# Kernel tuning notes

Measured on AMD Instinct MI355X. Metric: run time of the kernel, lower is better.

## Reference

```python
import jax, jax.numpy as jnp
import numpy as np

DENSE_SHAPE = (256, 3, 3, 256)  # (out_channels, kh, kw, in_channels)
STRIDES = (1, 1)


def _unfold_nchw(x, kh, kw, sh, sw):
    """torch.nn.functional.unfold layout: rows ordered (C, kh, kw)."""
    B, C, H, W = x.shape
    oh = (H - kh) // sh + 1
    ow = (W - kw) // sw + 1
    # [B, C, kh*kw, oh, ow]; small python loop over 3x3 kernel taps only
    patches = jnp.stack(
        [x[:, :, i:i + sh * oh:sh, j:j + sw * ow:sw]
         for i in range(kh) for j in range(kw)], axis=2)
    return patches.reshape(B, C * kh * kw, oh * ow), oh, ow


def setup_inputs() -> dict:
    key = jax.random.key(0)
    k1, k2, k3, k4, k5, k6 = jax.random.split(key, 6)
    O, kh, kw, C = DENSE_SHAPE
    nnz = 2048
    inp = jax.random.normal(k1, (4, 128, 128, C), dtype=jnp.float32)
    # per-column index ranges for COO weight indices [nnz, 4]
    io = jax.random.randint(k2, (nnz, 1), 0, O)
    ih = jax.random.randint(k3, (nnz, 1), 0, kh)
    iw = jax.random.randint(k4, (nnz, 1), 0, kw)
    ic = jax.random.randint(k5, (nnz, 1), 0, C)
    weight_indices = jnp.concatenate([io, ih, iw, ic], axis=1).astype(jnp.int64)
    weight_values = jax.random.normal(k6, (nnz,), dtype=jnp.float32)
    return {"input": inp, "weight_indices": weight_indices,
            "weight_values": weight_values}


def reference(input, weight_indices, weight_values):
    O, kh, kw, C = DENSE_SHAPE
    sh, sw = STRIDES
    B = input.shape[0]
    # densify COO weight (duplicates are summed, matching coalesce)
    W = jnp.zeros(DENSE_SHAPE, dtype=weight_values.dtype).at[
        weight_indices[:, 0], weight_indices[:, 1],
        weight_indices[:, 2], weight_indices[:, 3]].add(weight_values)
    x = jnp.transpose(input, (0, 3, 1, 2))  # NHWC -> NCHW
    U, oh, ow = _unfold_nchw(x, kh, kw, sh, sw)  # [B, C*kh*kw, oh*ow]
    # NOTE: faithful to the original: weight flattened in (kh,kw,C) order
    # while unfold rows are in (C,kh,kw) order -- same raw matmul.
    out = jnp.einsum('ok,bkl->bol', W.reshape(O, -1), U)
    out = out.reshape(B, O, oh, ow)
    return jnp.transpose(out, (0, 2, 3, 1))  # -> NHWC
```

## Files before the change

### kernel.cpp

```cpp
#include <hip/hip_runtime.h>
#include <cstdint>

#define H_IN   128
#define W_IN   128
#define C_IN   256
#define O_OUT  256
#define OH     126
#define OW     126

#define TY     8
#define TX     8
#define IR     (TY + 2)
#define ICOLS  (TX + 2)
#define NPIX   (IR * ICOLS)
#define COLB   516
#define ROWB   5264
#define IN_BYTES (9 * ROWB + 9 * COLB + COLB)
#define NWAVES 16
#define OPW    16
#define SST    18
#define STG_W  (64 * SST)
#define FLUSH_BYTES (8 * STG_W * 4)
#define LDS_BYTES IN_BYTES

__global__ void prep_kernel(const int* __restrict__ wi, const float* __restrict__ wv,
                            int nnz, int* __restrict__ sgS, int* __restrict__ sgBase,
                            int* __restrict__ perm, int2* __restrict__ tab) {
    __shared__ int cnt[256];
    __shared__ int ipos[256];
    __shared__ int prm[256];
    __shared__ int hist[64];
    __shared__ int hbase[65];
    __shared__ int hcur[64];
    __shared__ int smax[32];
    __shared__ int sbase[33];
    __shared__ int is32;
    const int tid = threadIdx.x;
    cnt[tid] = 0;
    if (tid < 64) { hist[tid] = 0; hcur[tid] = 0; }
    if (tid == 0) is32 = 0;
    __syncthreads();
    int f = 0;
    for (int idx = tid * 2 + 1; idx < nnz * 4; idx += 512) f |= wi[idx];
    if (f) atomicOr(&is32, 1);
    __syncthreads();
    const int stride = is32 ? 4 : 8;
    const int step   = is32 ? 1 : 2;
    for (int e = tid; e < nnz; e += 256)
        atomicAdd(&cnt[wi[e * stride]], 1);
    __syncthreads();
    { int key = 63 - min(cnt[tid], 63); atomicAdd(&hist[key], 1); }
    __syncthreads();
    if (tid == 0) {
        int s = 0;
        for (int i = 0; i < 64; ++i) { hbase[i] = s; s += hist[i]; }
        hbase[64] = s;
    }
    __syncthreads();
    { int key = 63 - min(cnt[tid], 63);
      int pos = hbase[key] + atomicAdd(&hcur[key], 1);
      ipos[tid] = pos; prm[pos] = tid; }
    __syncthreads();
    if (tid < 32) {
        int m = 0;
        for (int k = 0; k < 8; ++k) m = max(m, cnt[prm[tid * 8 + k]]);
        smax[tid] = m;
    }
    __syncthreads();
    if (tid == 0) {
        int s = 0;
        for (int i = 0; i < 32; ++i) { sbase[i] = s; s += 8 * smax[i]; }
        sbase[32] = s;
    }
    __syncthreads();
    const int T = sbase[32];
    for (int i = tid; i < T; i += 256) tab[i] = make_int2(0, 0);
    cnt[tid] = 0;
    __syncthreads();
    for (int e = tid; e < nnz; e += 256) {
        int o  = wi[e * stride];
        int h  = wi[e * stride + 1 * step];
        int w_ = wi[e * stride + 2 * step];
        int c  = wi[e * stride + 3 * step];
        int k   = h * 768 + w_ * 256 + c;
        int cp  = k / 9;
        int rem = k - cp * 9;
        int i_  = rem / 3;
        int j_  = rem - i_ * 3;
        int meta2 = i_ * ROWB + j_ * COLB + cp * 2;
        int slot = atomicAdd(&cnt[o], 1);
        int p    = ipos[o];
        tab[sbase[p >> 3] + slot * 8 + (p & 7)] = make_int2(meta2, __float_as_int(wv[e]));
    }
    if (tid < 32) sgS[tid] = smax[tid];
    if (tid < 33) sgBase[tid] = sbase[tid];
    perm[tid] = prm[tid];
}

__device__ inline unsigned short rtne_bf16(float f) {
    unsigned u = __float_as_uint(f);
    u += 0x7FFFu + ((u >> 16) & 1u);
    return (unsigned short)(u >> 16);
}

__device__ __forceinline__ float bfld(const char* b, int off) {
    return __uint_as_float(((unsigned)*(const unsigned short*)(b + off)) << 16);
}

__global__ __launch_bounds__(1024, 8)
void conv_kernel(const float* __restrict__ in, float* __restrict__ out,
                 const int* __restrict__ sgS, const int* __restrict__ sgBase,
                 const int* __restrict__ perm, const int2* __restrict__ tab) {
    extern __shared__ char smem[];
    float* ldsF = (float*)smem;

    const int tid  = threadIdx.x;
    const int w    = __builtin_amdgcn_readfirstlane(tid >> 6);
    const int lane = tid & 63;
    const int tx = blockIdx.x, ty = blockIdx.y, b = blockIdx.z;
    const int iy0 = ty * TY, ix0 = tx * TX;
    const float* inb = in + (size_t)b * (H_IN * W_IN * C_IN);

    for (int base = 0; base < 8; base += 4) {
        float4 v[4];
#pragma unroll
        for (int q = 0; q < 4; ++q) {
            int p = w + (base + q) * NWAVES;
            if (p < NPIX) {
                int r = p / ICOLS, c = p - r * ICOLS;
                int gy = iy0 + r, gx = ix0 + c;
                if (gy < H_IN && gx < W_IN)
                    v[q] = *(const float4*)(inb + ((gy * W_IN + gx) << 8) + (lane << 2));
            }
        }
#pragma unroll
        for (int q = 0; q < 4; ++q) {
            int p = w + (base + q) * NWAVES;
            if (p < NPIX) {
                int r = p / ICOLS, c = p - r * ICOLS;
                int gy = iy0 + r, gx = ix0 + c;
                if (gy < H_IN && gx < W_IN) {
                    ushort2 lo, hi;
                    lo.x = rtne_bf16(v[q].x); lo.y = rtne_bf16(v[q].y);
                    hi.x = rtne_bf16(v[q].z); hi.y = rtne_bf16(v[q].w);
                    unsigned short* d = (unsigned short*)(smem + r * ROWB + c * COLB) + (lane << 2);
                    *(ushort2*)(d)     = lo;
                    *(ushort2*)(d + 2) = hi;
                }
            }
        }
    }
    __syncthreads();

    const int A2  = (lane >> 3) * ROWB + (lane & 7) * COLB;
    const int g0 = w, g1 = 31 - w;
    const char* basep = (const char*)smem;
    float acc[OPW];
#pragma unroll
    for (int i = 0; i < OPW; ++i) acc[i] = 0.f;

#pragma unroll
    for (int g = 0; g < 2; ++g) {
        const int gi = g ? g1 : g0;
        const int S = sgS[gi];
        const int2* Tg = tab + sgBase[gi];
        for (int slot = 0; slot < S; ++slot) {
            const int4* R = (const int4*)(Tg + (slot << 3));
            const int4 p0 = R[0];
            const int4 p1 = R[1];
            const int4 p2 = R[2];
            const int4 p3 = R[3];
            acc[g * 8 + 0] += __int_as_float(p0.y) * bfld(basep, A2 + p0.x);
            acc[g * 8 + 1] += __int_as_float(p0.w) * bfld(basep, A2 + p0.z);
            acc[g * 8 + 2] += __int_as_float(p1.y) * bfld(basep, A2 + p1.x);
            acc[g * 8 + 3] += __int_as_float(p1.w) * bfld(basep, A2 + p1.z);
            acc[g * 8 + 4] += __int_as_float(p2.y) * bfld(basep, A2 + p2.x);
            acc[g * 8 + 5] += __int_as_float(p2.w) * bfld(basep, A2 + p2.z);
            acc[g * 8 + 6] += __int_as_float(p3.y) * bfld(basep, A2 + p3.x);
            acc[g * 8 + 7] += __int_as_float(p3.w) * bfld(basep, A2 + p3.z);
        }
    }

    __syncthreads();
    int tcs[OPW];
#pragma unroll
    for (int k = 0; k < OPW; ++k) {
        const int grp = (k < 8) ? g0 : g1;
        tcs[k] = perm[grp * 8 + (k & 7)];
    }
    const int ob = w * OPW;
#pragma unroll
    for (int k = 0; k < OPW; ++k) {
        const int tc = tcs[k];
        if ((tc >> 7) == 0)
            ldsF[((tc >> 4) & 7) * STG_W + lane * SST + (tc & 15)] = acc[k];
    }
    __syncthreads();
    if (w < 8) {
        const int a_  = lane >> 2;
        const int chq = lane & 3;
        const float* rb = ldsF + w * STG_W;
#pragma unroll
        for (int s16 = 0; s16 < 4; ++s16) {
            int p = s16 * 16 + a_;
            float2 u0 = *(const float2*)(rb + p * SST + chq * 4);
            float2 u1 = *(const float2*)(rb + p * SST + chq * 4 + 2);
            int poy = iy0 + (p >> 3), pox = ix0 + (p & 7);
            if (poy < OH && pox < OW) {
                float4 o4 = make_float4(u0.x, u0.y, u1.x, u1.y);
                *(float4*)(out + (((size_t)b * OH + poy) * OW + pox) * O_OUT + ob + chq * 4) = o4;
            }
        }
    }
    __syncthreads();
#pragma unroll
    for (int k = 0; k < OPW; ++k) {
        const int tc = tcs[k];
        if ((tc >> 7) == 1)
            ldsF[((tc >> 4) & 7) * STG_W + lane * SST + (tc & 15)] = acc[k];
    }
    __syncthreads();
    if (w >= 8) {
        const int a_  = lane >> 2;
        const int chq = lane & 3;
        const float* rb = ldsF + (w & 7) * STG_W;
#pragma unroll
        for (int s16 = 0; s16 < 4; ++s16) {
            int p = s16 * 16 + a_;
            float2 u0 = *(const float2*)(rb + p * SST + chq * 4);
            float2 u1 = *(const float2*)(rb + p * SST + chq * 4 + 2);
            int poy = iy0 + (p >> 3), pox = ix0 + (p & 7);
            if (poy < OH && pox < OW) {
                float4 o4 = make_float4(u0.x, u0.y, u1.x, u1.y);
                *(float4*)(out + (((size_t)b * OH + poy) * OW + pox) * O_OUT + ob + chq * 4) = o4;
            }
        }
    }
}

extern "C" void kernel_launch(void* const* d_in, const int* in_sizes, int n_in,
                              void* d_out, int out_size, void* d_ws, size_t ws_size,
                              hipStream_t stream) {
    const float* input = (const float*)d_in[0];
    const int*   widx  = (const int*)d_in[1];
    const float* wval  = (const float*)d_in[2];
    float* outp = (float*)d_out;
    const int nnz = in_sizes[2];
    const int B = in_sizes[0] / (H_IN * W_IN * C_IN);

    int*  sgS    = (int*)d_ws;
    int*  sgBase = sgS + 32;
    int*  perm   = (int*)((char*)d_ws + 512);
    int2* tab    = (int2*)((char*)d_ws + 2048);

    prep_kernel<<<1, 256, 0, stream>>>(widx, wval, nnz, sgS, sgBase, perm, tab);

    static_assert(LDS_BYTES >= FLUSH_BYTES, "flush pass must fit in input region");
    static_assert(2 * LDS_BYTES <= 160 * 1024, "need 2 blocks/CU");
    hipFuncSetAttribute((const void*)conv_kernel,
                        hipFuncAttributeMaxDynamicSharedMemorySize, LDS_BYTES);
    dim3 grid((OW + TX - 1) / TX, (OH + TY - 1) / TY, B);
    conv_kernel<<<grid, 1024, LDS_BYTES, stream>>>(input, outp, sgS, sgBase, perm, tab);
}
```

Baseline: 140.9 us.

## Swizzle block order, prefetch weight table rows, spread output flush across all waves

Remaps the flat block index so that consecutively launched blocks land on different batch and tile positions, changing L2 and channel locality. The sparse-weight table loop now software-prefetches the next slot's entries while computing the current one, hiding the table load latency behind LDS reads and FMAs. The output flush is restructured so all 16 waves write every stage instead of half idling, each lane storing two float4s per pixel. This adds register pressure from the prefetched int4s and relies on the swizzle matching the grid shape (16x16x4).

```diff
diff --git a/kernel.cpp b/kernel.cpp
--- a/kernel.cpp
+++ b/kernel.cpp
@@ -117,7 +117,9 @@
     const int tid  = threadIdx.x;
     const int w    = __builtin_amdgcn_readfirstlane(tid >> 6);
     const int lane = tid & 63;
-    const int tx = blockIdx.x, ty = blockIdx.y, b = blockIdx.z;
+    const int flat = ((int)blockIdx.z << 8) | ((int)blockIdx.y << 4) | (int)blockIdx.x;
+    const int swz  = ((flat & 7) << 7) | (flat >> 3);
+    const int tx = swz & 15, ty = (swz >> 4) & 15, b = swz >> 8;
     const int iy0 = ty * TY, ix0 = tx * TX;
     const float* inb = in + (size_t)b * (H_IN * W_IN * C_IN);
 
@@ -153,7 +155,6 @@
     __syncthreads();
 
     const int A2  = (lane >> 3) * ROWB + (lane & 7) * COLB;
-    const int g0 = w, g1 = 31 - w;
     const char* basep = (const char*)smem;
     float acc[OPW];
 #pragma unroll
@@ -161,23 +162,28 @@
 
 #pragma unroll
     for (int g = 0; g < 2; ++g) {
-        const int gi = g ? g1 : g0;
+        const int gi = g ? (31 - w) : w;
         const int S = sgS[gi];
-        const int2* Tg = tab + sgBase[gi];
-        for (int slot = 0; slot < S; ++slot) {
-            const int4* R = (const int4*)(Tg + (slot << 3));
-            const int4 p0 = R[0];
-            const int4 p1 = R[1];
-            const int4 p2 = R[2];
-            const int4 p3 = R[3];
-            acc[g * 8 + 0] += __int_as_float(p0.y) * bfld(basep, A2 + p0.x);
-            acc[g * 8 + 1] += __int_as_float(p0.w) * bfld(basep, A2 + p0.z);
-            acc[g * 8 + 2] += __int_as_float(p1.y) * bfld(basep, A2 + p1.x);
-            acc[g * 8 + 3] += __int_as_float(p1.w) * bfld(basep, A2 + p1.z);
-            acc[g * 8 + 4] += __int_as_float(p2.y) * bfld(basep, A2 + p2.x);
-            acc[g * 8 + 5] += __int_as_float(p2.w) * bfld(basep, A2 + p2.z);
-            acc[g * 8 + 6] += __int_as_float(p3.y) * bfld(basep, A2 + p3.x);
-            acc[g * 8 + 7] += __int_as_float(p3.w) * bfld(basep, A2 + p3.z);
+        if (S > 0) {
+            const int2* Tg = tab + sgBase[gi];
+            int4 c0 = ((const int4*)Tg)[0];
+            int4 c1 = ((const int4*)Tg)[1];
+            int4 c2 = ((const int4*)Tg)[2];
+            int4 c3 = ((const int4*)Tg)[3];
+            for (int slot = 0; slot < S; ++slot) {
+                const int nxt = (slot + 1 < S) ? (slot + 1) : slot;
+                const int4* Rn = (const int4*)(Tg + (nxt << 3));
+                int4 n0 = Rn[0], n1 = Rn[1], n2 = Rn[2], n3 = Rn[3];
+                acc[g * 8 + 0] += __int_as_float(c0.y) * bfld(basep, A2 + c0.x);
+                acc[g * 8 + 1] += __int_as_float(c0.w) * bfld(basep, A2 + c0.z);
+                acc[g * 8 + 2] += __int_as_float(c1.y) * bfld(basep, A2 + c1.x);
+                acc[g * 8 + 3] += __int_as_float(c1.w) * bfld(basep, A2 + c1.z);
+                acc[g * 8 + 4] += __int_as_float(c2.y) * bfld(basep, A2 + c2.x);
+                acc[g * 8 + 5] += __int_as_float(c2.w) * bfld(basep, A2 + c2.z);
+                acc[g * 8 + 6] += __int_as_float(c3.y) * bfld(basep, A2 + c3.x);
+                acc[g * 8 + 7] += __int_as_float(c3.w) * bfld(basep, A2 + c3.z);
+                c0 = n0; c1 = n1; c2 = n2; c3 = n3;
+            }
         }
     }
 
@@ -185,10 +191,16 @@
     int tcs[OPW];
 #pragma unroll
     for (int k = 0; k < OPW; ++k) {
-        const int grp = (k < 8) ? g0 : g1;
+        const int grp = (k < 8) ? w : (31 - w);
         tcs[k] = perm[grp * 8 + (k & 7)];
     }
-    const int ob = w * OPW;
+    const int rq   = w >> 1;
+    const int rpx  = (w & 1) * 32 + (lane >> 1);
+    const int half = lane & 1;
+    const int poy  = iy0 + (rpx >> 3), pox = ix0 + (rpx & 7);
+    const float* rb = ldsF + rq * STG_W + rpx * SST + half * 8;
+    float* outp0 = out + (((size_t)b * OH + poy) * OW + pox) * O_OUT + rq * 16 + half * 8;
+    const bool inb_px = (poy < OH) && (pox < OW);
 #pragma unroll
     for (int k = 0; k < OPW; ++k) {
         const int tc = tcs[k];
@@ -196,20 +208,14 @@
             ldsF[((tc >> 4) & 7) * STG_W + lane * SST + (tc & 15)] = acc[k];
     }
     __syncthreads();
-    if (w < 8) {
-        const int a_  = lane >> 2;
-        const int chq = lane & 3;
-        const float* rb = ldsF + w * STG_W;
-#pragma unroll
-        for (int s16 = 0; s16 < 4; ++s16) {
-            int p = s16 * 16 + a_;
-            float2 u0 = *(const float2*)(rb + p * SST + chq * 4);
-            float2 u1 = *(const float2*)(rb + p * SST + chq * 4 + 2);
-            int poy = iy0 + (p >> 3), pox = ix0 + (p & 7);
-            if (poy < OH && pox < OW) {
-                float4 o4 = make_float4(u0.x, u0.y, u1.x, u1.y);
-                *(float4*)(out + (((size_t)b * OH + poy) * OW + pox) * O_OUT + ob + chq * 4) = o4;
-            }
+    {
+        float2 u0 = *(const float2*)(rb + 0);
+        float2 u1 = *(const float2*)(rb + 2);
+        float2 u2 = *(const float2*)(rb + 4);
+        float2 u3 = *(const float2*)(rb + 6);
+        if (inb_px) {
+            *(float4*)(outp0 + 0) = make_float4(u0.x, u0.y, u1.x, u1.y);
+            *(float4*)(outp0 + 4) = make_float4(u2.x, u2.y, u3.x, u3.y);
         }
     }
     __syncthreads();
@@ -220,20 +226,14 @@
             ldsF[((tc >> 4) & 7) * STG_W + lane * SST + (tc & 15)] = acc[k];
     }
     __syncthreads();
-    if (w >= 8) {
-        const int a_  = lane >> 2;
-        const int chq = lane & 3;
-        const float* rb = ldsF + (w & 7) * STG_W;
-#pragma unroll
-        for (int s16 = 0; s16 < 4; ++s16) {
-            int p = s16 * 16 + a_;
-            float2 u0 = *(const float2*)(rb + p * SST + chq * 4);
-            float2 u1 = *(const float2*)(rb + p * SST + chq * 4 + 2);
-            int poy = iy0 + (p >> 3), pox = ix0 + (p & 7);
-            if (poy < OH && pox < OW) {
-                float4 o4 = make_float4(u0.x, u0.y, u1.x, u1.y);
-                *(float4*)(out + (((size_t)b * OH + poy) * OW + pox) * O_OUT + ob + chq * 4) = o4;
-            }
+    {
+        float2 u0 = *(const float2*)(rb + 0);
+        float2 u1 = *(const float2*)(rb + 2);
+        float2 u2 = *(const float2*)(rb + 4);
+        float2 u3 = *(const float2*)(rb + 6);
+        if (inb_px) {
+            *(float4*)(outp0 + 128 + 0) = make_float4(u0.x, u0.y, u1.x, u1.y);
+            *(float4*)(outp0 + 128 + 4) = make_float4(u2.x, u2.y, u3.x, u3.y);
         }
     }
 }
```

New measurement: 142.6 us. About the same (+1.2%).

## Single-pass output flush, swizzle block order, hoist permutation loads

Applied to the files above, without the earlier changes.

Replaces the two-phase staged output write with one pass: all 16 waves stage their accumulators into a larger LDS region (16 x 1156 floats), then each thread writes 64 contiguous bytes of one pixel's output. This removes two barriers and a serialized half-idle store phase. Block indices are remapped with a swizzle so consecutive blocks land on different tiles/batches, and the perm lookups are hoisted before the input load to hide their latency. LDS usage grows (~74KB per block), which still allows 2 blocks/CU but tightens the budget.

```diff
diff --git a/kernel.cpp b/kernel.cpp
--- a/kernel.cpp
+++ b/kernel.cpp
@@ -18,10 +18,10 @@
 #define IN_BYTES (9 * ROWB + 9 * COLB + COLB)
 #define NWAVES 16
 #define OPW    16
-#define SST    18
-#define STG_W  (64 * SST)
-#define FLUSH_BYTES (8 * STG_W * 4)
-#define LDS_BYTES IN_BYTES
+#define SSTW   18
+#define REGW   1156
+#define FLUSH_BYTES (16 * REGW * 4)
+#define LDS_BYTES FLUSH_BYTES
 
 __global__ void prep_kernel(const int* __restrict__ wi, const float* __restrict__ wv,
                             int nnz, int* __restrict__ sgS, int* __restrict__ sgBase,
@@ -117,9 +117,17 @@
     const int tid  = threadIdx.x;
     const int w    = __builtin_amdgcn_readfirstlane(tid >> 6);
     const int lane = tid & 63;
-    const int tx = blockIdx.x, ty = blockIdx.y, b = blockIdx.z;
+    const int flat = ((int)blockIdx.z << 8) | ((int)blockIdx.y << 4) | (int)blockIdx.x;
+    const int swz  = ((flat & 7) << 7) | (flat >> 3);
+    const int tx = swz & 15, ty = (swz >> 4) & 15, b = swz >> 8;
     const int iy0 = ty * TY, ix0 = tx * TX;
     const float* inb = in + (size_t)b * (H_IN * W_IN * C_IN);
+
+    const int g0 = w, g1 = 31 - w;
+    int tcs[OPW];
+#pragma unroll
+    for (int k = 0; k < OPW; ++k)
+        tcs[k] = perm[((k < 8) ? g0 : g1) * 8 + (k & 7)];
 
     for (int base = 0; base < 8; base += 4) {
         float4 v[4];
@@ -153,7 +161,6 @@
     __syncthreads();
 
     const int A2  = (lane >> 3) * ROWB + (lane & 7) * COLB;
-    const int g0 = w, g1 = 31 - w;
     const char* basep = (const char*)smem;
     float acc[OPW];
 #pragma unroll
@@ -182,58 +189,31 @@
     }
 
     __syncthreads();
-    int tcs[OPW];
-#pragma unroll
-    for (int k = 0; k < OPW; ++k) {
-        const int grp = (k < 8) ? g0 : g1;
-        tcs[k] = perm[grp * 8 + (k & 7)];
-    }
-    const int ob = w * OPW;
 #pragma unroll
     for (int k = 0; k < OPW; ++k) {
         const int tc = tcs[k];
-        if ((tc >> 7) == 0)
-            ldsF[((tc >> 4) & 7) * STG_W + lane * SST + (tc & 15)] = acc[k];
-    }
-    __syncthreads();
-    if (w < 8) {
-        const int a_  = lane >> 2;
-        const int chq = lane & 3;
-        const float* rb = ldsF + w * STG_W;
-#pragma unroll
-        for (int s16 = 0; s16 < 4; ++s16) {
-            int p = s16 * 16 + a_;
-            float2 u0 = *(const float2*)(rb + p * SST + chq * 4);
-            float2 u1 = *(const float2*)(rb + p * SST + chq * 4 + 2);
-            int poy = iy0 + (p >> 3), pox = ix0 + (p & 7);
-            if (poy < OH && pox < OW) {
-                float4 o4 = make_float4(u0.x, u0.y, u1.x, u1.y);
-                *(float4*)(out + (((size_t)b * OH + poy) * OW + pox) * O_OUT + ob + chq * 4) = o4;
-            }
-        }
-    }
-    __syncthreads();
-#pragma unroll
-    for (int k = 0; k < OPW; ++k) {
-        const int tc = tcs[k];
-        if ((tc >> 7) == 1)
-            ldsF[((tc >> 4) & 7) * STG_W + lane * SST + (tc & 15)] = acc[k];
-    }
-    __syncthreads();
-    if (w >= 8) {
-        const int a_  = lane >> 2;
-        const int chq = lane & 3;
-        const float* rb = ldsF + (w & 7) * STG_W;
-#pragma unroll
-        for (int s16 = 0; s16 < 4; ++s16) {
-            int p = s16 * 16 + a_;
-            float2 u0 = *(const float2*)(rb + p * SST + chq * 4);
-            float2 u1 = *(const float2*)(rb + p * SST + chq * 4 + 2);
-            int poy = iy0 + (p >> 3), pox = ix0 + (p & 7);
-            if (poy < OH && pox < OW) {
-                float4 o4 = make_float4(u0.x, u0.y, u1.x, u1.y);
-                *(float4*)(out + (((size_t)b * OH + poy) * OW + pox) * O_OUT + ob + chq * 4) = o4;
-            }
+        ldsF[(tc >> 4) * REGW + lane * SSTW + (tc & 15)] = acc[k];
+    }
+    __syncthreads();
+    {
+        const int px = tid >> 4;
+        const int q  = tid & 15;
+        const int poy = iy0 + (px >> 3), pox = ix0 + (px & 7);
+        if (poy < OH && pox < OW) {
+            const float* rb = ldsF + q * REGW + px * SSTW;
+            float2 u0 = *(const float2*)(rb + 0);
+            float2 u1 = *(const float2*)(rb + 2);
+            float2 u2 = *(const float2*)(rb + 4);
+            float2 u3 = *(const float2*)(rb + 6);
+            float2 u4 = *(const float2*)(rb + 8);
+            float2 u5 = *(const float2*)(rb + 10);
+            float2 u6 = *(const float2*)(rb + 12);
+            float2 u7 = *(const float2*)(rb + 14);
+            float* op = out + (((size_t)b * OH + poy) * OW + pox) * O_OUT + q * 16;
+            *(float4*)(op + 0)  = make_float4(u0.x, u0.y, u1.x, u1.y);
+            *(float4*)(op + 4)  = make_float4(u2.x, u2.y, u3.x, u3.y);
+            *(float4*)(op + 8)  = make_float4(u4.x, u4.y, u5.x, u5.y);
+            *(float4*)(op + 12) = make_float4(u6.x, u6.y, u7.x, u7.y);
         }
     }
 }
@@ -255,7 +235,7 @@
 
     prep_kernel<<<1, 256, 0, stream>>>(widx, wval, nnz, sgS, sgBase, perm, tab);
 
-    static_assert(LDS_BYTES >= FLUSH_BYTES, "flush pass must fit in input region");
+    static_assert(LDS_BYTES >= IN_BYTES, "flush region must cover input region");
     static_assert(2 * LDS_BYTES <= 160 * 1024, "need 2 blocks/CU");
     hipFuncSetAttribute((const void*)conv_kernel,
                         hipFuncAttributeMaxDynamicSharedMemorySize, LDS_BYTES);
```

New measurement: 147.3 us. 1.05x slower.
